# Kernel tuning notes

Hardware: AMD Instinct MI355X
Metric: run time of the kernel (lower is better)

The kernel has to match this reference:

```python
import jax, jax.numpy as jnp
import numpy as np

TAU = 2.0      # LIF time constant
EPS = 1e-5     # BatchNorm eps
ALPHA = 4.0    # sigmoid surrogate-gradient sharpness (spikingjelly default)

@jax.custom_vjp
def _spike(x):
    return (x >= 0.0).astype(x.dtype)

def _spike_fwd(x):
    return _spike(x), x

def _spike_bwd(x, g):
    s = jax.nn.sigmoid(ALPHA * x)
    return (g * ALPHA * s * (1.0 - s),)

_spike.defvjp(_spike_fwd, _spike_bwd)

def lif(x_seq, v_th=1.0):
    # Multi-step LIF with hard reset to 0, detach_reset=True, v[0]=0.
    # x_seq: (T, ...) ; scan over T.
    def step(v, x):
        v = v + (x - v) / TAU
        s = _spike(v - v_th)
        v = v * (1.0 - jax.lax.stop_gradient(s))  # detach_reset
        return v, s
    _, s_seq = jax.lax.scan(step, jnp.zeros_like(x_seq[0]), x_seq)
    return s_seq

def bn(x, gamma, beta, mean, var):
    # inference-mode BatchNorm2d on (T,B,C,H,W), params (C,)
    sh = (1, 1, -1, 1, 1)
    scale = gamma.reshape(sh) * jax.lax.rsqrt(var.reshape(sh) + EPS)
    return (x - mean.reshape(sh)) * scale + beta.reshape(sh)

def conv1x1(x, w):
    # 1x1 conv == channel matmul; x: (T,B,C,H,W), w: (Cout,Cin)
    return jnp.einsum('tbchw,dc->tbdhw', x, w)

def setup_inputs() -> dict:
    key = jax.random.key(0)
    ks = jax.random.split(key, 24)
    T, B, C, H, W = 4, 32, 384, 16, 16
    d = {}
    d['x'] = jax.random.normal(ks[0], (T, B, C, H, W), jnp.float32)
    for i, p in enumerate(['q', 'k', 'v']):
        base = 1 + 5 * i
        d[p + '_w'] = jax.random.normal(ks[base], (C, C), jnp.float32) * 0.05
        d[p + '_gamma'] = jax.random.uniform(ks[base + 1], (C,), jnp.float32) + 0.5
        d[p + '_beta'] = jax.random.normal(ks[base + 2], (C,), jnp.float32) * 0.1
        d[p + '_mean'] = jax.random.normal(ks[base + 3], (C,), jnp.float32) * 0.1
        d[p + '_var'] = jax.random.uniform(ks[base + 4], (C,), jnp.float32) + 0.5
    d['proj_w'] = jax.random.normal(ks[16], (C, C), jnp.float32) * 0.05
    d['proj_b'] = jax.random.normal(ks[17], (C,), jnp.float32) * 0.1
    d['proj_gamma'] = jax.random.uniform(ks[18], (C,), jnp.float32) + 0.5
    d['proj_beta'] = jax.random.normal(ks[19], (C,), jnp.float32) * 0.1
    d['proj_mean'] = jax.random.normal(ks[20], (C,), jnp.float32) * 0.1
    d['proj_var'] = jax.random.uniform(ks[21], (C,), jnp.float32) + 0.5
    d['num_heads'] = 8
    return d

def reference(x, q_w, q_gamma, q_beta, q_mean, q_var,
              k_w, k_gamma, k_beta, k_mean, k_var,
              v_w, v_gamma, v_beta, v_mean, v_var,
              proj_w, proj_b, proj_gamma, proj_beta, proj_mean, proj_var,
              num_heads):
    T, B, C, H, W = x.shape
    N = H * W
    Ch = C // num_heads
    identity = x
    xs = lif(x)  # shortcut_lif

    def branch(w, g, b, m, var_):
        o = lif(bn(conv1x1(xs, w), g, b, m, var_))  # (T,B,C,H,W), binary spikes
        # flatten(3).transpose(-1,-2).reshape(T,B,N,h,Ch).permute -> (T,B,h,N,Ch)
        return o.reshape(T, B, num_heads, Ch, N).transpose(0, 1, 2, 4, 3)

    q = branch(q_w, q_gamma, q_beta, q_mean, q_var)
    k = branch(k_w, k_gamma, k_beta, k_mean, k_var)
    v = branch(v_w, v_gamma, v_beta, v_mean, v_var)

    kv = (k * v).sum(axis=3, keepdims=True)      # (T,B,h,1,Ch) linear-attn reduce over N
    kv = lif(kv, v_th=0.5)                       # talking_heads_lif
    y = q * kv                                   # (T,B,h,N,Ch)
    y = y.transpose(0, 1, 2, 4, 3).reshape(T, B, C, H, W)
    y = conv1x1(y, proj_w) + proj_b.reshape(1, 1, -1, 1, 1)
    y = bn(y, proj_gamma, proj_beta, proj_mean, proj_var)
    return (y + identity, v)
```

## Files before the change

### kernel.cpp

```cpp
#include <hip/hip_runtime.h>

typedef unsigned short u16;
typedef unsigned char u8;
typedef signed char i8;
typedef int i32x4 __attribute__((ext_vector_type(4)));
typedef int i32x16 __attribute__((ext_vector_type(16)));
typedef u16 u16x8 __attribute__((ext_vector_type(8)));
typedef u8 u8x16 __attribute__((ext_vector_type(16)));

__device__ __forceinline__ void gload16(const void* g, void* l) {
    __builtin_amdgcn_global_load_lds(
        (const __attribute__((address_space(1))) void*)g,
        (__attribute__((address_space(3))) void*)l, 16, 0, 0);
}

__global__ __launch_bounds__(256) void prep(const float* __restrict__ X, u8* __restrict__ Xt,
    const float* __restrict__ qw, const float* __restrict__ kw,
    const float* __restrict__ vw, const float* __restrict__ pw,
    i8* __restrict__ Wq, float* __restrict__ Sc, float* __restrict__ KVraw) {
    const int bid = blockIdx.x;
    if (bid < 768) {
        __shared__ __attribute__((aligned(16))) u8 s2[4][32][136];
        const int c0 = (bid % 3) * 128;
        const int n0 = ((bid / 3) & 7) * 32;
        const int b = bid / 24;
        const int n_l = threadIdx.x & 31, cg = threadIdx.x >> 5;
        for (int jj = 0; jj < 16; jj++) {
            int c_l = cg + jj * 8;
            float vm = 0.f;
            #pragma unroll
            for (int t = 0; t < 4; t++) {
                float xv = X[(((long)t * 32 + b) * 384 + c0 + c_l) * 256 + n0 + n_l];
                vm += (xv - vm) * 0.5f;
                u8 sp = 0;
                if (vm >= 1.0f) { sp = 1; vm = 0.f; }
                s2[t][n_l][c_l] = sp;
            }
        }
        __syncthreads();
        const int c16 = (threadIdx.x & 7) << 4;
        const int n = (threadIdx.x >> 3) & 31;
        #pragma unroll
        for (int t = 0; t < 4; t++) {
            u8x16 v = *(const u8x16*)&s2[t][n][c16];
            *(u8x16*)&Xt[(((long)b * 256 + n0 + n) * 4 + t) * 384 + c0 + c16] = v;
        }
    } else {
        const int wv = bid - 768;
        const int w = threadIdx.x >> 6, lane = threadIdx.x & 63;
        const int r = wv * 4 + w;
        const int m = r / 384, d = r - m * 384;
        const float* srcs[4] = {qw, kw, vw, pw};
        const float* row = srcs[m] + (long)d * 384;
        float a[6]; float mx = 0.f;
        #pragma unroll
        for (int jj = 0; jj < 6; jj++) { a[jj] = row[lane + (jj << 6)]; mx = fmaxf(mx, fabsf(a[jj])); }
        #pragma unroll
        for (int off = 1; off < 64; off <<= 1) mx = fmaxf(mx, __shfl_xor(mx, off));
        float scale = mx * (1.f / 127.f);
        float sinv = mx > 0.f ? 127.f / mx : 0.f;
        if (lane == 0) Sc[r] = scale;
        i8* dst0 = Wq + (long)(m == 3 ? 9 : m * 3) * 147456 + (long)d * 384;
        #pragma unroll
        for (int jj = 0; jj < 6; jj++) {
            float x = a[jj] * sinv;
            float q1 = rintf(x);         float r1 = x - q1;
            float q2 = rintf(r1 * 128.f); float r2 = r1 * 128.f - q2;
            float q3 = rintf(r2 * 128.f);
            int c = lane + (jj << 6);
            dst0[c] = (i8)(int)q1;
            dst0[147456 + c] = (i8)(int)q2;
            if (m != 3) dst0[2 * 147456 + c] = (i8)(int)q3;
        }
        const int idx = wv * 256 + threadIdx.x;
        if (idx < 49152) KVraw[idx] = 0.f;
    }
}

template<int NL>
__device__ __forceinline__ void gemm_i8(const u8* __restrict__ A, const i8* __restrict__ B,
                                        long lstride, char* lds8, int m0, int n0, i32x16 (&acc)[NL][2][2]) {
    const int tid = threadIdx.x, l = tid & 63, w = tid >> 6;
    const int wm = (w & 1) << 6, wn = (w >> 1) << 6;
    const int col = l & 31, kg = l >> 5;
    const int r0 = tid >> 2, sl = tid & 3, r1 = r0 + 64;
    const int cs0 = (sl ^ ((r0 >> 1) & 3)) << 4;
    const int cs1 = (sl ^ ((r1 >> 1) & 3)) << 4;
    const u8* Ap0 = A + (long)(m0 + r0) * 384 + cs0;
    const u8* Ap1 = A + (long)(m0 + r1) * 384 + cs1;
    const i8* Bp0 = B + (long)(n0 + r0) * 384 + cs0;
    const i8* Bp1 = B + (long)(n0 + r1) * 384 + cs1;
    char* d0p = lds8 + r0 * 64 + sl * 16;
    char* d1p = lds8 + r1 * 64 + sl * 16;
    for (int kk = 0; kk < 384; kk += 64) {
        gload16(Ap0 + kk, d0p);
        gload16(Ap1 + kk, d1p);
        #pragma unroll
        for (int p = 0; p < NL; p++) {
            gload16(Bp0 + p * lstride + kk, d0p + (p + 1) * 8192);
            gload16(Bp1 + p * lstride + kk, d1p + (p + 1) * 8192);
        }
        __syncthreads();
        #pragma unroll
        for (int c = 0; c < 2; c++) {
            i32x4 af[2];
            #pragma unroll
            for (int i = 0; i < 2; i++) {
                int ra = wm + (i << 5) + col;
                int sa = ((2 * c + kg) ^ ((ra >> 1) & 3)) << 4;
                af[i] = *(const i32x4*)(lds8 + ra * 64 + sa);
            }
            #pragma unroll
            for (int p = 0; p < NL; p++)
                #pragma unroll
                for (int j = 0; j < 2; j++) {
                    int rb = wn + (j << 5) + col;
                    int sb = ((2 * c + kg) ^ ((rb >> 1) & 3)) << 4;
                    i32x4 bfr = *(const i32x4*)(lds8 + (p + 1) * 8192 + rb * 64 + sb);
                    #pragma unroll
                    for (int i = 0; i < 2; i++)
                        acc[p][i][j] = __builtin_amdgcn_mfma_i32_32x32x32_i8(af[i], bfr, acc[p][i][j], 0, 0, 0);
                }
        }
        __syncthreads();
    }
}

__global__ __launch_bounds__(256) void k2(
    const u8* __restrict__ Xt, const i8* __restrict__ Wq, const float* __restrict__ Sc,
    const float* __restrict__ g0, const float* __restrict__ b0, const float* __restrict__ m0_, const float* __restrict__ v0_,
    const float* __restrict__ g1, const float* __restrict__ b1, const float* __restrict__ m1_, const float* __restrict__ v1_,
    const float* __restrict__ g2, const float* __restrict__ b2, const float* __restrict__ m2_, const float* __restrict__ v2_,
    u8* __restrict__ oq, u8* __restrict__ ok, u8* __restrict__ ov, float* __restrict__ out1)
{
    __shared__ __attribute__((aligned(16))) char lds8[32768];
    const int bid = blockIdx.x;
    const int xcd = bid & 7, bi = bid >> 3;
    const int mt = (bi / 9) * 8 + xcd;
    const int sub = bi % 9;
    const int m0 = mt * 128, d0 = (sub % 3) * 128, br = sub / 3;
    const float* G  = br == 0 ? g0  : (br == 1 ? g1  : g2);
    const float* Be = br == 0 ? b0  : (br == 1 ? b1  : b2);
    const float* Mu = br == 0 ? m0_ : (br == 1 ? m1_ : m2_);
    const float* Va = br == 0 ? v0_ : (br == 1 ? v1_ : v2_);

    i32x16 acc[3][2][2];
    #pragma unroll
    for (int p = 0; p < 3; p++)
        #pragma unroll
        for (int i = 0; i < 2; i++)
            #pragma unroll
            for (int j = 0; j < 2; j++)
                #pragma unroll
                for (int r = 0; r < 16; r++) acc[p][i][j][r] = 0;
    gemm_i8<3>(Xt, Wq + (long)br * 3 * 147456, 147456L, lds8, m0, d0, acc);

    const int tid = threadIdx.x, l = tid & 63, w = tid >> 6;
    const int wm = (w & 1) << 6, wn = (w >> 1) << 6;
    const int col = l & 31;
    float scb[2], mu[2], be[2], wsc[2];
    #pragma unroll
    for (int j = 0; j < 2; j++) {
        int d = d0 + wn + (j << 5) + col;
        scb[j] = G[d] / sqrtf(Va[d] + 1e-5f);
        mu[j] = Mu[d];
        be[j] = Be[d];
        wsc[j] = Sc[br * 384 + d];
    }
    u8* tile8 = (u8*)lds8;
    const float c1 = 0.0078125f, c2 = 6.103515625e-05f;
    #pragma unroll
    for (int i = 0; i < 2; i++)
        #pragma unroll
        for (int j = 0; j < 2; j++)
            #pragma unroll
            for (int q = 0; q < 4; q++) {
                float vm = 0.f;
                int mb = wm + (i << 5) + (q << 3) + ((l >> 5) << 2);
                #pragma unroll
                for (int t = 0; t < 4; t++) {
                    int reg = q * 4 + t;
                    float f = (float)acc[0][i][j][reg] + (float)acc[1][i][j][reg] * c1
                            + (float)acc[2][i][j][reg] * c2;
                    float bn = (f * wsc[j] - mu[j]) * scb[j] + be[j];
                    vm += (bn - vm) * 0.5f;
                    u8 s = 0;
                    if (vm >= 1.0f) { s = 1; vm = 0.f; }
                    tile8[(mb + t) * 144 + wn + (j << 5) + col] = s;
                }
            }
    __syncthreads();
    const int c8 = (tid & 15) << 3;
    u8* Out8 = br == 0 ? oq : (br == 1 ? ok : ov);
    #pragma unroll
    for (int p = 0; p < 8; p++) {
        int ml = (tid >> 4) + (p << 4);
        *(uint2*)&Out8[(long)(m0 + ml) * 384 + d0 + c8] = *(const uint2*)&tile8[ml * 144 + c8];
    }
    if (br == 2) {
        const int b = m0 >> 10, n_base = (m0 >> 2) & 255;
        const int dl = tid & 127, d = d0 + dl;
        const int h = d / 48, ch = d % 48;
        for (int q = 0; q < 64; q++) {
            int ml = (tid >> 7) + (q << 1);
            int t = ml & 3, n = n_base + (ml >> 2);
            out1[((((long)t * 32 + b) * 8 + h) * 256 + n) * 48 + ch] =
                tile8[ml * 144 + dl] ? 1.0f : 0.f;
        }
    }
}

__global__ __launch_bounds__(384) void k3a(const u8* __restrict__ Ks, const u8* __restrict__ Vs,
                                           float* __restrict__ kv_raw) {
    const int b = blockIdx.y, nc = blockIdx.x;
    const int d4 = threadIdx.x * 4, t = threadIdx.y;
    int cnt0 = 0, cnt1 = 0, cnt2 = 0, cnt3 = 0;
    for (int nl = 0; nl < 32; nl++) {
        const long row = ((long)b * 256 + nc * 32 + nl) * 4 + t;
        uchar4 kk = *(const uchar4*)&Ks[row * 384 + d4];
        uchar4 vv = *(const uchar4*)&Vs[row * 384 + d4];
        cnt0 += (kk.x & vv.x); cnt1 += (kk.y & vv.y);
        cnt2 += (kk.z & vv.z); cnt3 += (kk.w & vv.w);
    }
    float* dst = &kv_raw[((long)t * 32 + b) * 384 + d4];
    atomicAdd(dst + 0, (float)cnt0);
    atomicAdd(dst + 1, (float)cnt1);
    atomicAdd(dst + 2, (float)cnt2);
    atomicAdd(dst + 3, (float)cnt3);
}

__global__ __launch_bounds__(384) void k3b(const float* __restrict__ kv_raw, u8* __restrict__ kvs) {
    const int b = blockIdx.x, d = threadIdx.x;
    float vm = 0.f;
    #pragma unroll
    for (int t = 0; t < 4; t++) {
        vm += (kv_raw[((long)t * 32 + b) * 384 + d] - vm) * 0.5f;
        u8 sp = 0;
        if (vm >= 0.5f) { sp = 1; vm = 0.f; }
        kvs[((long)t * 32 + b) * 384 + d] = sp;
    }
}

__global__ __launch_bounds__(256) void k3c(const u8* __restrict__ Qs, const u8* __restrict__ KVs,
                                           u8* __restrict__ Y) {
    const long i16 = ((long)blockIdx.x * 256 + threadIdx.x) * 16;
    const int m = (int)(i16 / 384), d16 = (int)(i16 % 384);
    const int t = m & 3, b = m >> 10;
    uint4 q = *(const uint4*)(Qs + i16);
    uint4 kvv = *(const uint4*)(KVs + ((long)(t * 32 + b) * 384 + d16));
    uint4 y;
    y.x = q.x & kvv.x; y.y = q.y & kvv.y; y.z = q.z & kvv.z; y.w = q.w & kvv.w;
    *(uint4*)(Y + i16) = y;
}

__global__ __launch_bounds__(256) void k4(
    const u8* __restrict__ Y, const i8* __restrict__ Pq, const float* __restrict__ Scp,
    const float* __restrict__ PB, const float* __restrict__ PG, const float* __restrict__ PBe,
    const float* __restrict__ PM, const float* __restrict__ PV,
    const float* __restrict__ X, float* __restrict__ O)
{
    __shared__ __attribute__((aligned(16))) char lds8[35072];
    const int bid = blockIdx.x;
    const int xcd = bid & 7, bi = bid >> 3;
    const int mt = (bi / 3) * 8 + xcd;
    const int m0 = mt * 128, e0 = (bi % 3) * 128;
    i32x16 acc[2][2][2];
    #pragma unroll
    for (int p = 0; p < 2; p++)
        #pragma unroll
        for (int i = 0; i < 2; i++)
            #pragma unroll
            for (int j = 0; j < 2; j++)
                #pragma unroll
                for (int r = 0; r < 16; r++) acc[p][i][j][r] = 0;
    gemm_i8<2>(Y, Pq, 147456L, lds8, m0, e0, acc);

    const int tid = threadIdx.x, l = tid & 63, w = tid >> 6;
    const int wm = (w & 1) << 6, wn = (w >> 1) << 6;
    const int col = l & 31;
    float scb[2], mu[2], be[2], pbb[2], wsc[2];
    #pragma unroll
    for (int j = 0; j < 2; j++) {
        int e = e0 + wn + (j << 5) + col;
        scb[j] = PG[e] / sqrtf(PV[e] + 1e-5f);
        mu[j] = PM[e];
        be[j] = PBe[e];
        pbb[j] = PB[e];
        wsc[j] = Scp[e];
    }
    float* smemf = (float*)lds8;
    const int b = m0 >> 10, n_base = (m0 >> 2) & 255;
    const float c1 = 0.0078125f;
    for (int cchunk = 0; cchunk < 2; cchunk++) {
        if ((w & 1) == cchunk) {
            #pragma unroll
            for (int i = 0; i < 2; i++)
                #pragma unroll
                for (int j = 0; j < 2; j++)
                    #pragma unroll
                    for (int q = 0; q < 4; q++)
                        #pragma unroll
                        for (int t = 0; t < 4; t++) {
                            int reg = q * 4 + t;
                            float f = (float)acc[0][i][j][reg] + (float)acc[1][i][j][reg] * c1;
                            float z = (f * wsc[j] + pbb[j] - mu[j]) * scb[j] + be[j];
                            smemf[((i << 5) + (q << 3) + ((l >> 5) << 2) + t) * 137 + wn + (j << 5) + col] = z;
                        }
        }
        __syncthreads();
        const int n_l = tid & 15, eg = tid >> 4;
        #pragma unroll
        for (int ee = 0; ee < 8; ee++) {
            int e_l = eg + (ee << 4);
            #pragma unroll
            for (int t = 0; t < 4; t++) {
                float z = smemf[((n_l << 2) + t) * 137 + e_l];
                long gi = (((long)t * 32 + b) * 384 + e0 + e_l) * 256 + n_base + (cchunk << 4) + n_l;
                O[gi] = z + X[gi];
            }
        }
        __syncthreads();
    }
}

extern "C" void kernel_launch(void* const* d_in, const int* in_sizes, int n_in,
                              void* d_out, int out_size, void* d_ws, size_t ws_size,
                              hipStream_t stream) {
    (void)in_sizes; (void)n_in; (void)out_size; (void)ws_size;
    const float* x   = (const float*)d_in[0];
    const float* qw  = (const float*)d_in[1];
    const float* qg  = (const float*)d_in[2];
    const float* qb  = (const float*)d_in[3];
    const float* qm  = (const float*)d_in[4];
    const float* qv  = (const float*)d_in[5];
    const float* kw  = (const float*)d_in[6];
    const float* kg  = (const float*)d_in[7];
    const float* kb  = (const float*)d_in[8];
    const float* km  = (const float*)d_in[9];
    const float* kv  = (const float*)d_in[10];
    const float* vw  = (const float*)d_in[11];
    const float* vg  = (const float*)d_in[12];
    const float* vb  = (const float*)d_in[13];
    const float* vm  = (const float*)d_in[14];
    const float* vv  = (const float*)d_in[15];
    const float* pw  = (const float*)d_in[16];
    const float* pb  = (const float*)d_in[17];
    const float* pg  = (const float*)d_in[18];
    const float* pbe = (const float*)d_in[19];
    const float* pm  = (const float*)d_in[20];
    const float* pv  = (const float*)d_in[21];

    float* out0 = (float*)d_out;
    float* out1 = out0 + 12582912;
    char*  ob   = (char*)d_out;
    u8*    Qs8  = (u8*)ob;
    u8*    Xt8  = (u8*)(ob + 12582912);
    char*  ws   = (char*)d_ws;
    u8*    Ks8  = (u8*)ws;
    u8*    Vs8  = (u8*)ws + 12582912;
    u8*    Yb8  = (u8*)ws;
    float* KVraw = (float*)(ws + 25165824);
    u8*    KVs8  = (u8*)(ws + 25362432);
    i8*    Wq    = (i8*)(ws + 25411584);
    float* Sc    = (float*)(ws + 27033600);

    hipLaunchKernelGGL(prep, dim3(1152), dim3(256), 0, stream, x, Xt8, qw, kw, vw, pw, Wq, Sc, KVraw);
    hipLaunchKernelGGL(k2, dim3(2304), dim3(256), 0, stream,
                       Xt8, Wq, Sc,
                       qg, qb, qm, qv,
                       kg, kb, km, kv,
                       vg, vb, vm, vv,
                       Qs8, Ks8, Vs8, out1);
    hipLaunchKernelGGL(k3a, dim3(8, 32), dim3(96, 4), 0, stream, Ks8, Vs8, KVraw);
    hipLaunchKernelGGL(k3b, dim3(32), dim3(384), 0, stream, KVraw, KVs8);
    hipLaunchKernelGGL(k3c, dim3(3072), dim3(256), 0, stream, Qs8, KVs8, Yb8);
    hipLaunchKernelGGL(k4, dim3(768), dim3(256), 0, stream,
                       Yb8, Wq + 9 * 147456L, Sc + 3 * 384, pb, pg, pbe, pm, pv, x, out0);
}
```

Before: 320.8 us.

## Halve GEMM N-tile to 64 in k2/k4 to double blocks and occupancy

```diff
diff --git a/kernel.cpp b/kernel.cpp
--- a/kernel.cpp
+++ b/kernel.cpp
@@ -5,6 +5,7 @@
 typedef signed char i8;
 typedef int i32x4 __attribute__((ext_vector_type(4)));
 typedef int i32x16 __attribute__((ext_vector_type(16)));
+typedef float f32x4 __attribute__((ext_vector_type(4)));
 typedef u16 u16x8 __attribute__((ext_vector_type(8)));
 typedef u8 u8x16 __attribute__((ext_vector_type(16)));
 
@@ -79,27 +80,21 @@
 
 template<int NL>
 __device__ __forceinline__ void gemm_i8(const u8* __restrict__ A, const i8* __restrict__ B,
-                                        long lstride, char* lds8, int m0, int n0, i32x16 (&acc)[NL][2][2]) {
+                                        long lstride, char* lds8, int m0, int n0, i32x16 (&acc)[NL][2]) {
     const int tid = threadIdx.x, l = tid & 63, w = tid >> 6;
-    const int wm = (w & 1) << 6, wn = (w >> 1) << 6;
+    const int wm = (w & 1) << 6, wn = (w >> 1) << 5;
     const int col = l & 31, kg = l >> 5;
-    const int r0 = tid >> 2, sl = tid & 3, r1 = r0 + 64;
-    const int cs0 = (sl ^ ((r0 >> 1) & 3)) << 4;
-    const int cs1 = (sl ^ ((r1 >> 1) & 3)) << 4;
-    const u8* Ap0 = A + (long)(m0 + r0) * 384 + cs0;
-    const u8* Ap1 = A + (long)(m0 + r1) * 384 + cs1;
-    const i8* Bp0 = B + (long)(n0 + r0) * 384 + cs0;
-    const i8* Bp1 = B + (long)(n0 + r1) * 384 + cs1;
-    char* d0p = lds8 + r0 * 64 + sl * 16;
-    char* d1p = lds8 + r1 * 64 + sl * 16;
+    const int rA = tid >> 2, sl = tid & 3;
+    const int cs = (sl ^ ((rA >> 1) & 3)) << 4;
+    const u8* Ap = A + (long)(m0 + rA) * 384 + cs;
+    const i8* Bp = B + (long)(n0 + rA) * 384 + cs;
+    char* dst = lds8 + tid * 16;
     for (int kk = 0; kk < 384; kk += 64) {
-        gload16(Ap0 + kk, d0p);
-        gload16(Ap1 + kk, d1p);
-        #pragma unroll
-        for (int p = 0; p < NL; p++) {
-            gload16(Bp0 + p * lstride + kk, d0p + (p + 1) * 8192);
-            gload16(Bp1 + p * lstride + kk, d1p + (p + 1) * 8192);
-        }
+        gload16(Ap + kk, dst);
+        gload16(Ap + 24576 + kk, dst + 4096);
+        #pragma unroll
+        for (int p = 0; p < NL; p++)
+            gload16(Bp + p * lstride + kk, dst + 8192 + p * 4096);
         __syncthreads();
         #pragma unroll
         for (int c = 0; c < 2; c++) {
@@ -110,102 +105,90 @@
                 int sa = ((2 * c + kg) ^ ((ra >> 1) & 3)) << 4;
                 af[i] = *(const i32x4*)(lds8 + ra * 64 + sa);
             }
-            #pragma unroll
-            for (int p = 0; p < NL; p++)
+            int rb = wn + col;
+            int sb = ((2 * c + kg) ^ ((rb >> 1) & 3)) << 4;
+            #pragma unroll
+            for (int p = 0; p < NL; p++) {
+                i32x4 bf = *(const i32x4*)(lds8 + 8192 + p * 4096 + rb * 64 + sb);
                 #pragma unroll
-                for (int j = 0; j < 2; j++) {
-                    int rb = wn + (j << 5) + col;
-                    int sb = ((2 * c + kg) ^ ((rb >> 1) & 3)) << 4;
-                    i32x4 bfr = *(const i32x4*)(lds8 + (p + 1) * 8192 + rb * 64 + sb);
-                    #pragma unroll
-                    for (int i = 0; i < 2; i++)
-                        acc[p][i][j] = __builtin_amdgcn_mfma_i32_32x32x32_i8(af[i], bfr, acc[p][i][j], 0, 0, 0);
-                }
+                for (int i = 0; i < 2; i++)
+                    acc[p][i] = __builtin_amdgcn_mfma_i32_32x32x32_i8(af[i], bf, acc[p][i], 0, 0, 0);
+            }
         }
         __syncthreads();
     }
 }
 
-__global__ __launch_bounds__(256) void k2(
+__global__ __launch_bounds__(256, 4) void k2(
     const u8* __restrict__ Xt, const i8* __restrict__ Wq, const float* __restrict__ Sc,
     const float* __restrict__ g0, const float* __restrict__ b0, const float* __restrict__ m0_, const float* __restrict__ v0_,
     const float* __restrict__ g1, const float* __restrict__ b1, const float* __restrict__ m1_, const float* __restrict__ v1_,
     const float* __restrict__ g2, const float* __restrict__ b2, const float* __restrict__ m2_, const float* __restrict__ v2_,
     u8* __restrict__ oq, u8* __restrict__ ok, u8* __restrict__ ov, float* __restrict__ out1)
 {
-    __shared__ __attribute__((aligned(16))) char lds8[32768];
+    __shared__ __attribute__((aligned(16))) char lds8[20480];
     const int bid = blockIdx.x;
     const int xcd = bid & 7, bi = bid >> 3;
-    const int mt = (bi / 9) * 8 + xcd;
-    const int sub = bi % 9;
-    const int m0 = mt * 128, d0 = (sub % 3) * 128, br = sub / 3;
+    const int mt = (bi / 18) * 8 + xcd;
+    const int sub = bi % 18;
+    const int m0 = mt * 128, d0 = (sub % 6) * 64, br = sub / 6;
     const float* G  = br == 0 ? g0  : (br == 1 ? g1  : g2);
     const float* Be = br == 0 ? b0  : (br == 1 ? b1  : b2);
     const float* Mu = br == 0 ? m0_ : (br == 1 ? m1_ : m2_);
     const float* Va = br == 0 ? v0_ : (br == 1 ? v1_ : v2_);
 
-    i32x16 acc[3][2][2];
+    i32x16 acc[3][2];
     #pragma unroll
     for (int p = 0; p < 3; p++)
         #pragma unroll
         for (int i = 0; i < 2; i++)
             #pragma unroll
-            for (int j = 0; j < 2; j++)
-                #pragma unroll
-                for (int r = 0; r < 16; r++) acc[p][i][j][r] = 0;
+            for (int r = 0; r < 16; r++) acc[p][i][r] = 0;
     gemm_i8<3>(Xt, Wq + (long)br * 3 * 147456, 147456L, lds8, m0, d0, acc);
 
     const int tid = threadIdx.x, l = tid & 63, w = tid >> 6;
-    const int wm = (w & 1) << 6, wn = (w >> 1) << 6;
+    const int wm = (w & 1) << 6, wn = (w >> 1) << 5;
     const int col = l & 31;
-    float scb[2], mu[2], be[2], wsc[2];
-    #pragma unroll
-    for (int j = 0; j < 2; j++) {
-        int d = d0 + wn + (j << 5) + col;
-        scb[j] = G[d] / sqrtf(Va[d] + 1e-5f);
-        mu[j] = Mu[d];
-        be[j] = Be[d];
-        wsc[j] = Sc[br * 384 + d];
-    }
+    const int d = d0 + wn + col;
+    const float scb = G[d] / sqrtf(Va[d] + 1e-5f);
+    const float mu = Mu[d], be = Be[d];
+    const float wsc = Sc[br * 384 + d];
     u8* tile8 = (u8*)lds8;
     const float c1 = 0.0078125f, c2 = 6.103515625e-05f;
     #pragma unroll
     for (int i = 0; i < 2; i++)
         #pragma unroll
-        for (int j = 0; j < 2; j++)
-            #pragma unroll
-            for (int q = 0; q < 4; q++) {
-                float vm = 0.f;
-                int mb = wm + (i << 5) + (q << 3) + ((l >> 5) << 2);
-                #pragma unroll
-                for (int t = 0; t < 4; t++) {
-                    int reg = q * 4 + t;
-                    float f = (float)acc[0][i][j][reg] + (float)acc[1][i][j][reg] * c1
-                            + (float)acc[2][i][j][reg] * c2;
-                    float bn = (f * wsc[j] - mu[j]) * scb[j] + be[j];
-                    vm += (bn - vm) * 0.5f;
-                    u8 s = 0;
-                    if (vm >= 1.0f) { s = 1; vm = 0.f; }
-                    tile8[(mb + t) * 144 + wn + (j << 5) + col] = s;
-                }
-            }
+        for (int q = 0; q < 4; q++) {
+            float vm = 0.f;
+            int mb = wm + (i << 5) + (q << 3) + ((l >> 5) << 2);
+            #pragma unroll
+            for (int t = 0; t < 4; t++) {
+                int reg = q * 4 + t;
+                float f = (float)acc[0][i][reg] + (float)acc[1][i][reg] * c1
+                        + (float)acc[2][i][reg] * c2;
+                float bn = (f * wsc - mu) * scb + be;
+                vm += (bn - vm) * 0.5f;
+                u8 s = 0;
+                if (vm >= 1.0f) { s = 1; vm = 0.f; }
+                tile8[(mb + t) * 80 + wn + col] = s;
+            }
+        }
     __syncthreads();
-    const int c8 = (tid & 15) << 3;
+    const int ml = tid >> 1, cb = (tid & 1) << 5;
     u8* Out8 = br == 0 ? oq : (br == 1 ? ok : ov);
-    #pragma unroll
-    for (int p = 0; p < 8; p++) {
-        int ml = (tid >> 4) + (p << 4);
-        *(uint2*)&Out8[(long)(m0 + ml) * 384 + d0 + c8] = *(const uint2*)&tile8[ml * 144 + c8];
-    }
+    uint4 w0 = *(const uint4*)&tile8[ml * 80 + cb];
+    uint4 w1 = *(const uint4*)&tile8[ml * 80 + cb + 16];
+    *(uint4*)&Out8[(long)(m0 + ml) * 384 + d0 + cb] = w0;
+    *(uint4*)&Out8[(long)(m0 + ml) * 384 + d0 + cb + 16] = w1;
     if (br == 2) {
         const int b = m0 >> 10, n_base = (m0 >> 2) & 255;
-        const int dl = tid & 127, d = d0 + dl;
-        const int h = d / 48, ch = d % 48;
-        for (int q = 0; q < 64; q++) {
-            int ml = (tid >> 7) + (q << 1);
-            int t = ml & 3, n = n_base + (ml >> 2);
+        const int dl = tid & 63, d2 = d0 + dl;
+        const int h = d2 / 48, ch = d2 % 48;
+        for (int q = 0; q < 32; q++) {
+            int mlq = (tid >> 6) + (q << 2);
+            int t = mlq & 3, n = n_base + (mlq >> 2);
             out1[((((long)t * 32 + b) * 8 + h) * 256 + n) * 48 + ch] =
-                tile8[ml * 144 + dl] ? 1.0f : 0.f;
+                tile8[mlq * 80 + dl] ? 1.0f : 0.f;
         }
     }
 }
@@ -253,73 +236,59 @@
     *(uint4*)(Y + i16) = y;
 }
 
-__global__ __launch_bounds__(256) void k4(
+__global__ __launch_bounds__(256, 4) void k4(
     const u8* __restrict__ Y, const i8* __restrict__ Pq, const float* __restrict__ Scp,
     const float* __restrict__ PB, const float* __restrict__ PG, const float* __restrict__ PBe,
     const float* __restrict__ PM, const float* __restrict__ PV,
     const float* __restrict__ X, float* __restrict__ O)
 {
-    __shared__ __attribute__((aligned(16))) char lds8[35072];
+    __shared__ __attribute__((aligned(16))) char lds8[33792];
     const int bid = blockIdx.x;
     const int xcd = bid & 7, bi = bid >> 3;
-    const int mt = (bi / 3) * 8 + xcd;
-    const int m0 = mt * 128, e0 = (bi % 3) * 128;
-    i32x16 acc[2][2][2];
+    const int mt = (bi / 6) * 8 + xcd;
+    const int m0 = mt * 128, e0 = (bi % 6) * 64;
+    i32x16 acc[2][2];
     #pragma unroll
     for (int p = 0; p < 2; p++)
         #pragma unroll
         for (int i = 0; i < 2; i++)
             #pragma unroll
-            for (int j = 0; j < 2; j++)
-                #pragma unroll
-                for (int r = 0; r < 16; r++) acc[p][i][j][r] = 0;
+            for (int r = 0; r < 16; r++) acc[p][i][r] = 0;
     gemm_i8<2>(Y, Pq, 147456L, lds8, m0, e0, acc);
 
     const int tid = threadIdx.x, l = tid & 63, w = tid >> 6;
-    const int wm = (w & 1) << 6, wn = (w >> 1) << 6;
+    const int wm = (w & 1) << 6, wn = (w >> 1) << 5;
     const int col = l & 31;
-    float scb[2], mu[2], be[2], pbb[2], wsc[2];
-    #pragma unroll
-    for (int j = 0; j < 2; j++) {
-        int e = e0 + wn + (j << 5) + col;
-        scb[j] = PG[e] / sqrtf(PV[e] + 1e-5f);
-        mu[j] = PM[e];
-        be[j] = PBe[e];
-        pbb[j] = PB[e];
-        wsc[j] = Scp[e];
-    }
+    const int e = e0 + wn + col;
+    const float scb = PG[e] / sqrtf(PV[e] + 1e-5f);
+    const float mu = PM[e], be = PBe[e], pbb = PB[e];
+    const float wsc = Scp[e];
     float* smemf = (float*)lds8;
+    const float c1 = 0.0078125f;
+    #pragma unroll
+    for (int i = 0; i < 2; i++)
+        #pragma unroll
+        for (int q = 0; q < 4; q++)
+            #pragma unroll
+            for (int t = 0; t < 4; t++) {
+                int reg = q * 4 + t;
+                float f = (float)acc[0][i][reg] + (float)acc[1][i][reg] * c1;
+                float z = (f * wsc + pbb - mu) * scb + be;
+                int m = wm + (i << 5) + (q << 3) + ((l >> 5) << 2) + t;
+                smemf[(wn + col) * 132 + m] = z;
+            }
+    __syncthreads();
     const int b = m0 >> 10, n_base = (m0 >> 2) & 255;
-    const float c1 = 0.0078125f;
-    for (int cchunk = 0; cchunk < 2; cchunk++) {
-        if ((w & 1) == cchunk) {
-            #pragma unroll
-            for (int i = 0; i < 2; i++)
-                #pragma unroll
-                for (int j = 0; j < 2; j++)
-                    #pragma unroll
-                    for (int q = 0; q < 4; q++)
-                        #pragma unroll
-                        for (int t = 0; t < 4; t++) {
-                            int reg = q * 4 + t;
-                            float f = (float)acc[0][i][j][reg] + (float)acc[1][i][j][reg] * c1;
-                            float z = (f * wsc[j] + pbb[j] - mu[j]) * scb[j] + be[j];
-                            smemf[((i << 5) + (q << 3) + ((l >> 5) << 2) + t) * 137 + wn + (j << 5) + col] = z;
-                        }
-        }
-        __syncthreads();
-        const int n_l = tid & 15, eg = tid >> 4;
-        #pragma unroll
-        for (int ee = 0; ee < 8; ee++) {
-            int e_l = eg + (ee << 4);
-            #pragma unroll
-            for (int t = 0; t < 4; t++) {
-                float z = smemf[((n_l << 2) + t) * 137 + e_l];
-                long gi = (((long)t * 32 + b) * 384 + e0 + e_l) * 256 + n_base + (cchunk << 4) + n_l;
-                O[gi] = z + X[gi];
-            }
-        }
-        __syncthreads();
+    const int n_l = tid & 31;
+    #pragma unroll
+    for (int ei = 0; ei < 8; ei++) {
+        int e_l = (tid >> 5) + (ei << 3);
+        f32x4 v = *(const f32x4*)&smemf[e_l * 132 + (n_l << 2)];
+        #pragma unroll
+        for (int t = 0; t < 4; t++) {
+            long gi = (((long)t * 32 + b) * 384 + e0 + e_l) * 256 + n_base + n_l;
+            O[gi] = v[t] + X[gi];
+        }
     }
 }
 
@@ -365,7 +334,7 @@
     float* Sc    = (float*)(ws + 27033600);
 
     hipLaunchKernelGGL(prep, dim3(1152), dim3(256), 0, stream, x, Xt8, qw, kw, vw, pw, Wq, Sc, KVraw);
-    hipLaunchKernelGGL(k2, dim3(2304), dim3(256), 0, stream,
+    hipLaunchKernelGGL(k2, dim3(4608), dim3(256), 0, stream,
                        Xt8, Wq, Sc,
                        qg, qb, qm, qv,
                        kg, kb, km, kv,
@@ -374,6 +343,6 @@
     hipLaunchKernelGGL(k3a, dim3(8, 32), dim3(96, 4), 0, stream, Ks8, Vs8, KVraw);
     hipLaunchKernelGGL(k3b, dim3(32), dim3(384), 0, stream, KVraw, KVs8);
     hipLaunchKernelGGL(k3c, dim3(3072), dim3(256), 0, stream, Qs8, KVs8, Yb8);
-    hipLaunchKernelGGL(k4, dim3(768), dim3(256), 0, stream,
+    hipLaunchKernelGGL(k4, dim3(768 * 2), dim3(256), 0, stream,
                        Yb8, Wq + 9 * 147456L, Sc + 3 * 384, pb, pg, pbe, pm, pv, x, out0);
 }
```

Result: faster. 286.9 us (-10.6%).
